# Kernel optimization log

Measured on AMD Instinct MI355X. Metric: run time of the kernel, lower is better.

## Reference

```python
import jax, jax.numpy as jnp
import numpy as np

N = 100000      # nodes
E = 1600000     # nonzeros in sparse H (avg degree 16)
IN_DIM = 128
HID = 128
OUT = 128


def setup_inputs() -> dict:
    key = jax.random.key(0)
    k = jax.random.split(key, 8)
    X = jax.random.normal(k[0], (N, IN_DIM), dtype=jnp.float32)
    H_rows = jax.random.randint(k[1], (E,), 0, N, dtype=jnp.int32)
    H_cols = jax.random.randint(k[2], (E,), 0, N, dtype=jnp.int32)
    H_vals = jax.random.uniform(k[3], (E,), dtype=jnp.float32)
    # Linear params (PyTorch: y = x @ W.T + b); store as [in, out] for x @ W
    s1 = 1.0 / np.sqrt(IN_DIM)
    s2 = 1.0 / np.sqrt(HID)
    W1 = jax.random.uniform(k[4], (IN_DIM, HID), jnp.float32, -s1, s1)
    b1 = jax.random.uniform(k[5], (HID,), jnp.float32, -s1, s1)
    W2 = jax.random.uniform(k[6], (HID, OUT), jnp.float32, -s2, s2)
    b2 = jax.random.uniform(k[7], (OUT,), jnp.float32, -s2, s2)
    return {"X": X, "H_rows": H_rows, "H_cols": H_cols, "H_vals": H_vals,
            "W1": W1, "b1": b1, "W2": W2, "b2": b2}


def _spmm(rows, cols, vals, X):
    # sparse [N,N] @ dense [N,d] via edge gather + segment-sum
    msgs = vals[:, None] * X[cols]            # [E, d]
    return jax.ops.segment_sum(msgs, rows, num_segments=N)


def reference(X, H_rows, H_cols, H_vals, W1, b1, W2, b2):
    # num_layers == 2 branch; dropout is identity (eval mode)
    h = _spmm(H_rows, H_cols, H_vals, X @ W1 + b1)   # H @ W1(X)
    h = jax.nn.relu(h)
    out = _spmm(H_rows, H_cols, H_vals, h @ W2 + b2) # H @ W2(h)
    return out
```

## Files before the change

kernel.cpp:

```cpp
#include <hip/hip_runtime.h>

#define NNODES 100000
#define DIM 128
#define BROWS 256
#define NB ((NNODES + BROWS - 1) / BROWS)
#define BCAP 5120
#define CHUNK 4096

typedef _Float16 half8 __attribute__((ext_vector_type(8)));
typedef float f32x4 __attribute__((ext_vector_type(4)));

__device__ __forceinline__ unsigned int pack_bf16x2(float lo, float hi) {
    unsigned int ul = __float_as_uint(lo);
    unsigned int uh = __float_as_uint(hi);
    ul = (ul + 0x7fffu + ((ul >> 16) & 1u)) >> 16;
    uh = (uh + 0x7fffu + ((uh >> 16) & 1u)) & 0xffff0000u;
    return uh | ul;
}

__device__ __forceinline__ void unpack_bf16x8(uint4 v, float* f) {
    f[0] = __uint_as_float(v.x << 16); f[1] = __uint_as_float(v.x & 0xffff0000u);
    f[2] = __uint_as_float(v.y << 16); f[3] = __uint_as_float(v.y & 0xffff0000u);
    f[4] = __uint_as_float(v.z << 16); f[5] = __uint_as_float(v.z & 0xffff0000u);
    f[6] = __uint_as_float(v.w << 16); f[7] = __uint_as_float(v.w & 0xffff0000u);
}

__global__ __launch_bounds__(256) void prep_w(const float* __restrict__ W1s,
                                              const float* __restrict__ W2s,
                                              _Float16* __restrict__ Wt1,
                                              _Float16* __restrict__ Wt2) {
    const int b = blockIdx.x;
    const float* __restrict__ W = (b & 4) ? W2s : W1s;
    _Float16* __restrict__ Wt = (b & 4) ? Wt2 : Wt1;
    const int base = (b & 3) * 4096;
    for (int i = threadIdx.x; i < 4096; i += 256) {
        const int e = base + i;
        const int k = e >> 7, c = e & 127;
        Wt[c * 128 + k] = (_Float16)W[e];
    }
}

template <bool IN_BF16>
__global__ __launch_bounds__(256) void gemm_mfma(const void* __restrict__ Ain,
                                                 const _Float16* __restrict__ Wt,
                                                 const float* __restrict__ bias,
                                                 unsigned short* __restrict__ Yb, int n) {
    const int t = threadIdx.x;
    const int l = t & 63;
    const int lr = l & 15;
    const int lg = l >> 4;
    const int r0 = blockIdx.x * 128 + (t >> 6) * 32;

    half8 xf[2][4];
#pragma unroll
    for (int rt = 0; rt < 2; ++rt) {
        const int row = r0 + rt * 16 + lr;
        const bool ok = row < n;
        if (IN_BF16) {
            const uint4* __restrict__ A16 = (const uint4*)Ain;
#pragma unroll
            for (int ks = 0; ks < 4; ++ks) {
                uint4 v = make_uint4(0u, 0u, 0u, 0u);
                if (ok) v = A16[(size_t)row * 16 + ks * 4 + lg];
                float f[8];
                unpack_bf16x8(v, f);
                half8 h;
#pragma unroll
                for (int j = 0; j < 8; ++j) h[j] = (_Float16)f[j];
                xf[rt][ks] = h;
            }
        } else {
            const float4* __restrict__ A4 = (const float4*)Ain;
#pragma unroll
            for (int ks = 0; ks < 4; ++ks) {
                float4 v0 = make_float4(0.f, 0.f, 0.f, 0.f);
                float4 v1 = v0;
                if (ok) {
                    v0 = A4[(size_t)row * 32 + ks * 8 + lg * 2];
                    v1 = A4[(size_t)row * 32 + ks * 8 + lg * 2 + 1];
                }
                half8 h;
                h[0] = (_Float16)v0.x; h[1] = (_Float16)v0.y;
                h[2] = (_Float16)v0.z; h[3] = (_Float16)v0.w;
                h[4] = (_Float16)v1.x; h[5] = (_Float16)v1.y;
                h[6] = (_Float16)v1.z; h[7] = (_Float16)v1.w;
                xf[rt][ks] = h;
            }
        }
    }

    const f32x4 zero4 = {0.f, 0.f, 0.f, 0.f};
    f32x4 acc[2][8];
#pragma unroll
    for (int rt = 0; rt < 2; ++rt)
#pragma unroll
        for (int ct = 0; ct < 8; ++ct) acc[rt][ct] = zero4;

    const half8* __restrict__ Wf = (const half8*)Wt;
#pragma unroll
    for (int ct = 0; ct < 8; ++ct) {
        half8 wf[4];
#pragma unroll
        for (int ks = 0; ks < 4; ++ks)
            wf[ks] = Wf[(ct * 16 + lr) * 16 + ks * 4 + lg];
#pragma unroll
        for (int ks = 0; ks < 4; ++ks) {
            acc[0][ct] = __builtin_amdgcn_mfma_f32_16x16x32_f16(wf[ks], xf[0][ks], acc[0][ct], 0, 0, 0);
            acc[1][ct] = __builtin_amdgcn_mfma_f32_16x16x32_f16(wf[ks], xf[1][ks], acc[1][ct], 0, 0, 0);
        }
    }

#pragma unroll
    for (int ct = 0; ct < 8; ++ct) {
        const int c0 = ct * 16 + lg * 4;
        const float4 bv = *(const float4*)&bias[c0];
#pragma unroll
        for (int rt = 0; rt < 2; ++rt) {
            const int row = r0 + rt * 16 + lr;
            if (row < n) {
                f32x4 a = acc[rt][ct];
                uint2 pv = make_uint2(pack_bf16x2(a[0] + bv.x, a[1] + bv.y),
                                      pack_bf16x2(a[2] + bv.z, a[3] + bv.w));
                *(uint2*)&Yb[(size_t)row * DIM + c0] = pv;
            }
        }
    }
}

__global__ __launch_bounds__(256) void pass1_bin(const int* __restrict__ rows,
                                                 const int* __restrict__ cols,
                                                 const float* __restrict__ vals,
                                                 int* __restrict__ bcnt,
                                                 int2* __restrict__ tmp, int nnz) {
    __shared__ int hist[NB];
    __shared__ int base[NB];
    __shared__ int cur[NB];
    const int t = threadIdx.x;
    const int e0 = blockIdx.x * CHUNK;
    const int e1 = min(e0 + CHUNK, nnz);

    for (int i = t; i < NB; i += 256) { hist[i] = 0; cur[i] = 0; }
    __syncthreads();

    for (int i = e0 + t; i < e1; i += 256)
        atomicAdd(&hist[rows[i] >> 8], 1);
    __syncthreads();

    for (int i = t; i < NB; i += 256)
        base[i] = (hist[i] > 0) ? atomicAdd(&bcnt[i], hist[i]) : 0;
    __syncthreads();

    for (int i = e0 + t; i < e1; i += 256) {
        const int r = rows[i];
        const int b = r >> 8;
        const int pos = base[b] + atomicAdd(&cur[b], 1);
        if (pos < BCAP)
            tmp[(size_t)b * BCAP + pos] =
                make_int2(((r & 255) << 24) | cols[i], __float_as_int(vals[i]));
    }
}

__global__ __launch_bounds__(256) void pass2_sort(const int2* __restrict__ tmp,
                                                  const int* __restrict__ bcnt,
                                                  int2* __restrict__ epack,
                                                  int* __restrict__ row_ptr,
                                                  int* __restrict__ counts, int n) {
    __shared__ int2 ebuf[BCAP];
    __shared__ int cnt[256];
    __shared__ int s[256];
    __shared__ int cur[256];
    const int b = blockIdx.x;
    const int t = threadIdx.x;
    const int row0 = b * BROWS;
    const int nrows = min(BROWS, n - row0);
    const int m = min(bcnt[b], BCAP);
    const int2* __restrict__ src = tmp + (size_t)b * BCAP;

    int partial = 0;
    for (int i = t; i < b; i += 256) partial += bcnt[i];
    s[t] = partial;
    __syncthreads();
    for (int off = 128; off >= 1; off >>= 1) {
        if (t < off) s[t] += s[t + off];
        __syncthreads();
    }
    const int base = s[0];
    __syncthreads();

    cnt[t] = 0;
    __syncthreads();
    for (int i = t; i < m; i += 256)
        atomicAdd(&cnt[((unsigned)src[i].x) >> 24], 1);
    __syncthreads();

    const int v = cnt[t];
    s[t] = v;
    __syncthreads();
    for (int off = 1; off < 256; off <<= 1) {
        int x = (t >= off) ? s[t - off] : 0;
        __syncthreads();
        s[t] += x;
        __syncthreads();
    }
    const int excl = s[t] - v;
    if (t < nrows) {
        row_ptr[row0 + t] = base + excl;
        counts[row0 + t] = v;
    }
    cur[t] = excl;
    __syncthreads();

    for (int i = t; i < m; i += 256) {
        const int2 e = src[i];
        const int rl = ((unsigned)e.x) >> 24;
        const int pos = atomicAdd(&cur[rl], 1);
        ebuf[pos] = make_int2(e.x & 0xFFFFFF, e.y);
    }
    __syncthreads();

    {
        const int lo = excl;
        const int hi = s[t];
        for (int i = lo + 1; i < hi; ++i) {
            int2 key = ebuf[i];
            int j = i - 1;
            while (j >= lo && ebuf[j].x > key.x) { ebuf[j + 1] = ebuf[j]; --j; }
            ebuf[j + 1] = key;
        }
    }
    __syncthreads();

    for (int i = t; i < m; i += 256)
        epack[base + i] = ebuf[i];
}

template <bool RELU_OUT, bool OUT_BF16>
__global__ __launch_bounds__(256) void spmm_csr(const int* __restrict__ row_ptr,
                                                const int* __restrict__ counts,
                                                const int2* __restrict__ epack,
                                                const unsigned short* __restrict__ Xb,
                                                void* __restrict__ out, int n) {
    const int gid = blockIdx.x * blockDim.x + threadIdx.x;
    const int r = gid >> 4;
    const int lane = gid & 15;
    if (r >= n) return;
    const int start = row_ptr[r];
    const int cnt = counts[r];
    const uint4* __restrict__ X16 = (const uint4*)Xb;
    const int2* __restrict__ ep = epack + start;

    float acc[8];
#pragma unroll
    for (int k = 0; k < 8; ++k) acc[k] = 0.f;

    int j = 0;
    for (; j + 4 <= cnt; j += 4) {
        const int2 e0 = ep[j], e1 = ep[j + 1], e2 = ep[j + 2], e3 = ep[j + 3];
        const uint4 x0 = X16[(size_t)e0.x * 16 + lane];
        const uint4 x1 = X16[(size_t)e1.x * 16 + lane];
        const uint4 x2 = X16[(size_t)e2.x * 16 + lane];
        const uint4 x3 = X16[(size_t)e3.x * 16 + lane];
        const float v0 = __int_as_float(e0.y), v1 = __int_as_float(e1.y);
        const float v2 = __int_as_float(e2.y), v3 = __int_as_float(e3.y);
        float f0[8], f1[8], f2[8], f3[8];
        unpack_bf16x8(x0, f0); unpack_bf16x8(x1, f1);
        unpack_bf16x8(x2, f2); unpack_bf16x8(x3, f3);
#pragma unroll
        for (int k = 0; k < 8; ++k)
            acc[k] += v0 * f0[k] + v1 * f1[k] + v2 * f2[k] + v3 * f3[k];
    }
    for (; j < cnt; ++j) {
        const int2 e = ep[j];
        const uint4 x = X16[(size_t)e.x * 16 + lane];
        const float v = __int_as_float(e.y);
        float f[8];
        unpack_bf16x8(x, f);
#pragma unroll
        for (int k = 0; k < 8; ++k) acc[k] += v * f[k];
    }

    if (RELU_OUT) {
#pragma unroll
        for (int k = 0; k < 8; ++k) acc[k] = fmaxf(acc[k], 0.f);
    }

    if (OUT_BF16) {
        uint4 pv = make_uint4(pack_bf16x2(acc[0], acc[1]), pack_bf16x2(acc[2], acc[3]),
                              pack_bf16x2(acc[4], acc[5]), pack_bf16x2(acc[6], acc[7]));
        ((uint4*)out)[(size_t)r * 16 + lane] = pv;
    } else {
        float* of = (float*)out;
        *(float4*)&of[(size_t)r * DIM + lane * 8]     = make_float4(acc[0], acc[1], acc[2], acc[3]);
        *(float4*)&of[(size_t)r * DIM + lane * 8 + 4] = make_float4(acc[4], acc[5], acc[6], acc[7]);
    }
}

extern "C" void kernel_launch(void* const* d_in, const int* in_sizes, int n_in,
                              void* d_out, int out_size, void* d_ws, size_t ws_size,
                              hipStream_t stream) {
    const float* X      = (const float*)d_in[0];
    const int*   H_rows = (const int*)d_in[1];
    const int*   H_cols = (const int*)d_in[2];
    const float* H_vals = (const float*)d_in[3];
    const float* W1     = (const float*)d_in[4];
    const float* b1     = (const float*)d_in[5];
    const float* W2     = (const float*)d_in[6];
    const float* b2     = (const float*)d_in[7];
    float* out = (float*)d_out;

    const int E = in_sizes[1];
    const int N = NNODES;
    const size_t bmat_bytes = (size_t)N * DIM * 2;

    const int gemm_blocks = (N + 127) / 128;
    const int p1_blocks = (E + CHUNK - 1) / CHUNK;
    const int spmm_blocks = (N * 16 + 255) / 256;

    char* p = (char*)d_ws;
    unsigned short* Yb = (unsigned short*)p;  p += bmat_bytes;
    unsigned short* hb = (unsigned short*)p;  p += bmat_bytes;
    _Float16* Wt1      = (_Float16*)p;        p += 128 * 128 * 2;
    _Float16* Wt2      = (_Float16*)p;        p += 128 * 128 * 2;
    int2* epack        = (int2*)p;            p += (size_t)E * 8;
    int2* tmp          = (int2*)p;            p += (size_t)NB * BCAP * 8;
    int*  bcnt         = (int*)p;             p += (size_t)NB * 4;
    int*  row_ptr      = (int*)p;             p += (size_t)N * 4;
    int*  counts       = (int*)p;             p += (size_t)N * 4;

    prep_w<<<8, 256, 0, stream>>>(W1, W2, Wt1, Wt2);

    hipMemsetAsync(bcnt, 0, (size_t)NB * 4, stream);
    pass1_bin<<<p1_blocks, 256, 0, stream>>>(H_rows, H_cols, H_vals, bcnt, tmp, E);
    pass2_sort<<<NB, 256, 0, stream>>>(tmp, bcnt, epack, row_ptr, counts, N);

    gemm_mfma<false><<<gemm_blocks, 256, 0, stream>>>(X, Wt1, b1, Yb, N);
    spmm_csr<true, true><<<spmm_blocks, 256, 0, stream>>>(row_ptr, counts, epack, Yb, hb, N);

    gemm_mfma<true><<<gemm_blocks, 256, 0, stream>>>(hb, Wt2, b2, Yb, N);
    spmm_csr<false, false><<<spmm_blocks, 256, 0, stream>>>(row_ptr, counts, epack, Yb, out, N);
}
```

Measured before the change: 405.7 us.

## Merge weight prep and GEMM1 into binning kernels, drop per-row sort, add nontemporal hints

Weight transposition now runs as extra blocks of the binning kernel, and the first GEMM runs as extra blocks of the bucket-scatter kernel, which cuts two launches and lets independent work overlap. The per-row insertion sort through shared memory is removed, so edges are scattered straight to the global CSR array in atomic order. That changes the summation order within a row but not the result beyond rounding. Nontemporal loads and stores are added for streaming edge, input and output traffic so they pollute the cache less, which leaves the gathered feature rows more room in cache.

```diff
diff --git a/kernel.cpp b/kernel.cpp
--- a/kernel.cpp
+++ b/kernel.cpp
@@ -9,6 +9,8 @@
 
 typedef _Float16 half8 __attribute__((ext_vector_type(8)));
 typedef float f32x4 __attribute__((ext_vector_type(4)));
+typedef unsigned int u32x4 __attribute__((ext_vector_type(4)));
+typedef unsigned long long u64;
 
 __device__ __forceinline__ unsigned int pack_bf16x2(float lo, float hi) {
     unsigned int ul = __float_as_uint(lo);
@@ -18,38 +20,23 @@
     return uh | ul;
 }
 
-__device__ __forceinline__ void unpack_bf16x8(uint4 v, float* f) {
+__device__ __forceinline__ void unpack_bf16x8_v(u32x4 v, float* f) {
     f[0] = __uint_as_float(v.x << 16); f[1] = __uint_as_float(v.x & 0xffff0000u);
     f[2] = __uint_as_float(v.y << 16); f[3] = __uint_as_float(v.y & 0xffff0000u);
     f[4] = __uint_as_float(v.z << 16); f[5] = __uint_as_float(v.z & 0xffff0000u);
     f[6] = __uint_as_float(v.w << 16); f[7] = __uint_as_float(v.w & 0xffff0000u);
 }
 
-__global__ __launch_bounds__(256) void prep_w(const float* __restrict__ W1s,
-                                              const float* __restrict__ W2s,
-                                              _Float16* __restrict__ Wt1,
-                                              _Float16* __restrict__ Wt2) {
-    const int b = blockIdx.x;
-    const float* __restrict__ W = (b & 4) ? W2s : W1s;
-    _Float16* __restrict__ Wt = (b & 4) ? Wt2 : Wt1;
-    const int base = (b & 3) * 4096;
-    for (int i = threadIdx.x; i < 4096; i += 256) {
-        const int e = base + i;
-        const int k = e >> 7, c = e & 127;
-        Wt[c * 128 + k] = (_Float16)W[e];
-    }
-}
-
 template <bool IN_BF16>
-__global__ __launch_bounds__(256) void gemm_mfma(const void* __restrict__ Ain,
-                                                 const _Float16* __restrict__ Wt,
-                                                 const float* __restrict__ bias,
-                                                 unsigned short* __restrict__ Yb, int n) {
+__device__ __forceinline__ void gemm_body(int blk, const void* __restrict__ Ain,
+                                          const _Float16* __restrict__ Wt,
+                                          const float* __restrict__ bias,
+                                          unsigned short* __restrict__ Yb, int n) {
     const int t = threadIdx.x;
     const int l = t & 63;
     const int lr = l & 15;
     const int lg = l >> 4;
-    const int r0 = blockIdx.x * 128 + (t >> 6) * 32;
+    const int r0 = blk * 128 + (t >> 6) * 32;
 
     half8 xf[2][4];
 #pragma unroll
@@ -57,27 +44,27 @@
         const int row = r0 + rt * 16 + lr;
         const bool ok = row < n;
         if (IN_BF16) {
-            const uint4* __restrict__ A16 = (const uint4*)Ain;
+            const u32x4* __restrict__ A16 = (const u32x4*)Ain;
 #pragma unroll
             for (int ks = 0; ks < 4; ++ks) {
-                uint4 v = make_uint4(0u, 0u, 0u, 0u);
-                if (ok) v = A16[(size_t)row * 16 + ks * 4 + lg];
+                u32x4 v = {0u, 0u, 0u, 0u};
+                if (ok) v = __builtin_nontemporal_load(&A16[(size_t)row * 16 + ks * 4 + lg]);
                 float f[8];
-                unpack_bf16x8(v, f);
+                unpack_bf16x8_v(v, f);
                 half8 h;
 #pragma unroll
                 for (int j = 0; j < 8; ++j) h[j] = (_Float16)f[j];
                 xf[rt][ks] = h;
             }
         } else {
-            const float4* __restrict__ A4 = (const float4*)Ain;
+            const f32x4* __restrict__ A4 = (const f32x4*)Ain;
 #pragma unroll
             for (int ks = 0; ks < 4; ++ks) {
-                float4 v0 = make_float4(0.f, 0.f, 0.f, 0.f);
-                float4 v1 = v0;
+                f32x4 v0 = {0.f, 0.f, 0.f, 0.f};
+                f32x4 v1 = v0;
                 if (ok) {
-                    v0 = A4[(size_t)row * 32 + ks * 8 + lg * 2];
-                    v1 = A4[(size_t)row * 32 + ks * 8 + lg * 2 + 1];
+                    v0 = __builtin_nontemporal_load(&A4[(size_t)row * 32 + ks * 8 + lg * 2]);
+                    v1 = __builtin_nontemporal_load(&A4[(size_t)row * 32 + ks * 8 + lg * 2 + 1]);
                 }
                 half8 h;
                 h[0] = (_Float16)v0.x; h[1] = (_Float16)v0.y;
@@ -119,23 +106,49 @@
             const int row = r0 + rt * 16 + lr;
             if (row < n) {
                 f32x4 a = acc[rt][ct];
-                uint2 pv = make_uint2(pack_bf16x2(a[0] + bv.x, a[1] + bv.y),
-                                      pack_bf16x2(a[2] + bv.z, a[3] + bv.w));
+                const uint2 pv = make_uint2(pack_bf16x2(a[0] + bv.x, a[1] + bv.y),
+                                            pack_bf16x2(a[2] + bv.z, a[3] + bv.w));
                 *(uint2*)&Yb[(size_t)row * DIM + c0] = pv;
             }
         }
     }
+}
+
+__global__ __launch_bounds__(256) void gemm_mfma_bf16(const void* __restrict__ Ain,
+                                                      const _Float16* __restrict__ Wt,
+                                                      const float* __restrict__ bias,
+                                                      unsigned short* __restrict__ Yb, int n) {
+    gemm_body<true>(blockIdx.x, Ain, Wt, bias, Yb, n);
 }
 
 __global__ __launch_bounds__(256) void pass1_bin(const int* __restrict__ rows,
                                                  const int* __restrict__ cols,
                                                  const float* __restrict__ vals,
                                                  int* __restrict__ bcnt,
-                                                 int2* __restrict__ tmp, int nnz) {
+                                                 int2* __restrict__ tmp, int nnz,
+                                                 int p1_blocks,
+                                                 const float* __restrict__ W1s,
+                                                 const float* __restrict__ W2s,
+                                                 _Float16* __restrict__ Wt1,
+                                                 _Float16* __restrict__ Wt2) {
     __shared__ int hist[NB];
     __shared__ int base[NB];
     __shared__ int cur[NB];
     const int t = threadIdx.x;
+
+    if (blockIdx.x >= (unsigned)p1_blocks) {
+        const int b = blockIdx.x - p1_blocks;
+        const float* __restrict__ W = (b & 4) ? W2s : W1s;
+        _Float16* __restrict__ Wt = (b & 4) ? Wt2 : Wt1;
+        const int base2 = (b & 3) * 4096;
+        for (int i = t; i < 4096; i += 256) {
+            const int e = base2 + i;
+            const int k = e >> 7, c = e & 127;
+            Wt[c * 128 + k] = (_Float16)W[e];
+        }
+        return;
+    }
+
     const int e0 = blockIdx.x * CHUNK;
     const int e1 = min(e0 + CHUNK, nnz);
 
@@ -160,15 +173,24 @@
     }
 }
 
-__global__ __launch_bounds__(256) void pass2_sort(const int2* __restrict__ tmp,
-                                                  const int* __restrict__ bcnt,
-                                                  int2* __restrict__ epack,
-                                                  int* __restrict__ row_ptr,
-                                                  int* __restrict__ counts, int n) {
-    __shared__ int2 ebuf[BCAP];
+__global__ __launch_bounds__(256) void pass2_gemm1(const int2* __restrict__ tmp,
+                                                   const int* __restrict__ bcnt,
+                                                   int2* __restrict__ epack,
+                                                   int* __restrict__ row_ptr,
+                                                   int* __restrict__ counts,
+                                                   const float* __restrict__ X,
+                                                   const _Float16* __restrict__ Wt1,
+                                                   const float* __restrict__ b1,
+                                                   unsigned short* __restrict__ Yb, int n) {
     __shared__ int cnt[256];
     __shared__ int s[256];
     __shared__ int cur[256];
+
+    if (blockIdx.x >= NB) {
+        gemm_body<false>(blockIdx.x - NB, X, Wt1, b1, Yb, n);
+        return;
+    }
+
     const int b = blockIdx.x;
     const int t = threadIdx.x;
     const int row0 = b * BROWS;
@@ -207,31 +229,15 @@
         row_ptr[row0 + t] = base + excl;
         counts[row0 + t] = v;
     }
-    cur[t] = excl;
+    cur[t] = base + excl;
     __syncthreads();
 
     for (int i = t; i < m; i += 256) {
         const int2 e = src[i];
         const int rl = ((unsigned)e.x) >> 24;
         const int pos = atomicAdd(&cur[rl], 1);
-        ebuf[pos] = make_int2(e.x & 0xFFFFFF, e.y);
-    }
-    __syncthreads();
-
-    {
-        const int lo = excl;
-        const int hi = s[t];
-        for (int i = lo + 1; i < hi; ++i) {
-            int2 key = ebuf[i];
-            int j = i - 1;
-            while (j >= lo && ebuf[j].x > key.x) { ebuf[j + 1] = ebuf[j]; --j; }
-            ebuf[j + 1] = key;
-        }
-    }
-    __syncthreads();
-
-    for (int i = t; i < m; i += 256)
-        epack[base + i] = ebuf[i];
+        epack[pos] = make_int2(e.x & 0xFFFFFF, e.y);
+    }
 }
 
 template <bool RELU_OUT, bool OUT_BF16>
@@ -246,8 +252,8 @@
     if (r >= n) return;
     const int start = row_ptr[r];
     const int cnt = counts[r];
-    const uint4* __restrict__ X16 = (const uint4*)Xb;
-    const int2* __restrict__ ep = epack + start;
+    const u32x4* __restrict__ X16 = (const u32x4*)Xb;
+    const u64* __restrict__ ep = (const u64*)(epack + start);
 
     float acc[8];
 #pragma unroll
@@ -255,26 +261,31 @@
 
     int j = 0;
     for (; j + 4 <= cnt; j += 4) {
-        const int2 e0 = ep[j], e1 = ep[j + 1], e2 = ep[j + 2], e3 = ep[j + 3];
-        const uint4 x0 = X16[(size_t)e0.x * 16 + lane];
-        const uint4 x1 = X16[(size_t)e1.x * 16 + lane];
-        const uint4 x2 = X16[(size_t)e2.x * 16 + lane];
-        const uint4 x3 = X16[(size_t)e3.x * 16 + lane];
-        const float v0 = __int_as_float(e0.y), v1 = __int_as_float(e1.y);
-        const float v2 = __int_as_float(e2.y), v3 = __int_as_float(e3.y);
+        const u64 e0 = __builtin_nontemporal_load(&ep[j]);
+        const u64 e1 = __builtin_nontemporal_load(&ep[j + 1]);
+        const u64 e2 = __builtin_nontemporal_load(&ep[j + 2]);
+        const u64 e3 = __builtin_nontemporal_load(&ep[j + 3]);
+        const u32x4 x0 = X16[(size_t)(unsigned)(e0 & 0xffffffffu) * 16 + lane];
+        const u32x4 x1 = X16[(size_t)(unsigned)(e1 & 0xffffffffu) * 16 + lane];
+        const u32x4 x2 = X16[(size_t)(unsigned)(e2 & 0xffffffffu) * 16 + lane];
+        const u32x4 x3 = X16[(size_t)(unsigned)(e3 & 0xffffffffu) * 16 + lane];
+        const float v0 = __uint_as_float((unsigned)(e0 >> 32));
+        const float v1 = __uint_as_float((unsigned)(e1 >> 32));
+        const float v2 = __uint_as_float((unsigned)(e2 >> 32));
+        const float v3 = __uint_as_float((unsigned)(e3 >> 32));
         float f0[8], f1[8], f2[8], f3[8];
-        unpack_bf16x8(x0, f0); unpack_bf16x8(x1, f1);
-        unpack_bf16x8(x2, f2); unpack_bf16x8(x3, f3);
+        unpack_bf16x8_v(x0, f0); unpack_bf16x8_v(x1, f1);
+        unpack_bf16x8_v(x2, f2); unpack_bf16x8_v(x3, f3);
 #pragma unroll
         for (int k = 0; k < 8; ++k)
             acc[k] += v0 * f0[k] + v1 * f1[k] + v2 * f2[k] + v3 * f3[k];
     }
     for (; j < cnt; ++j) {
-        const int2 e = ep[j];
-        const uint4 x = X16[(size_t)e.x * 16 + lane];
-        const float v = __int_as_float(e.y);
+        const u64 e = __builtin_nontemporal_load(&ep[j]);
+        const u32x4 x = X16[(size_t)(unsigned)(e & 0xffffffffu) * 16 + lane];
+        const float v = __uint_as_float((unsigned)(e >> 32));
         float f[8];
-        unpack_bf16x8(x, f);
+        unpack_bf16x8_v(x, f);
 #pragma unroll
         for (int k = 0; k < 8; ++k) acc[k] += v * f[k];
     }
@@ -285,13 +296,16 @@
     }
 
     if (OUT_BF16) {
-        uint4 pv = make_uint4(pack_bf16x2(acc[0], acc[1]), pack_bf16x2(acc[2], acc[3]),
-                              pack_bf16x2(acc[4], acc[5]), pack_bf16x2(acc[6], acc[7]));
-        ((uint4*)out)[(size_t)r * 16 + lane] = pv;
+        u32x4 pv;
+        pv.x = pack_bf16x2(acc[0], acc[1]); pv.y = pack_bf16x2(acc[2], acc[3]);
+        pv.z = pack_bf16x2(acc[4], acc[5]); pv.w = pack_bf16x2(acc[6], acc[7]);
+        __builtin_nontemporal_store(pv, (u32x4*)out + (size_t)r * 16 + lane);
     } else {
         float* of = (float*)out;
-        *(float4*)&of[(size_t)r * DIM + lane * 8]     = make_float4(acc[0], acc[1], acc[2], acc[3]);
-        *(float4*)&of[(size_t)r * DIM + lane * 8 + 4] = make_float4(acc[4], acc[5], acc[6], acc[7]);
+        f32x4 a0 = {acc[0], acc[1], acc[2], acc[3]};
+        f32x4 a1 = {acc[4], acc[5], acc[6], acc[7]};
+        __builtin_nontemporal_store(a0, (f32x4*)&of[(size_t)r * DIM + lane * 8]);
+        __builtin_nontemporal_store(a1, (f32x4*)&of[(size_t)r * DIM + lane * 8 + 4]);
     }
 }
 
@@ -327,15 +341,15 @@
     int*  row_ptr      = (int*)p;             p += (size_t)N * 4;
     int*  counts       = (int*)p;             p += (size_t)N * 4;
 
-    prep_w<<<8, 256, 0, stream>>>(W1, W2, Wt1, Wt2);
-
     hipMemsetAsync(bcnt, 0, (size_t)NB * 4, stream);
-    pass1_bin<<<p1_blocks, 256, 0, stream>>>(H_rows, H_cols, H_vals, bcnt, tmp, E);
-    pass2_sort<<<NB, 256, 0, stream>>>(tmp, bcnt, epack, row_ptr, counts, N);
-
-    gemm_mfma<false><<<gemm_blocks, 256, 0, stream>>>(X, Wt1, b1, Yb, N);
+    pass1_bin<<<p1_blocks + 8, 256, 0, stream>>>(H_rows, H_cols, H_vals, bcnt, tmp, E,
+                                                 p1_blocks, W1, W2, Wt1, Wt2);
+
+    pass2_gemm1<<<NB + gemm_blocks, 256, 0, stream>>>(tmp, bcnt, epack, row_ptr, counts,
+                                                      X, Wt1, b1, Yb, N);
+
     spmm_csr<true, true><<<spmm_blocks, 256, 0, stream>>>(row_ptr, counts, epack, Yb, hb, N);
 
-    gemm_mfma<true><<<gemm_blocks, 256, 0, stream>>>(hb, Wt2, b2, Yb, N);
+    gemm_mfma_bf16<<<gemm_blocks, 256, 0, stream>>>(hb, Wt2, b2, Yb, N);
     spmm_csr<false, false><<<spmm_blocks, 256, 0, stream>>>(row_ptr, counts, epack, Yb, out, N);
 }
```

Result: faster. 365.2 us (-10.0%).
